# Optimization experiments

Measured on AMD Instinct MI355X. Metric: run time of the kernel, lower is better.

Reference implementation:

```python
import jax, jax.numpy as jnp
import numpy as np

# dims
B, T = 32, 512            # batch (cells), num TFs
G, PPG = 2000, 10         # num genes, cCRE peaks per gene (uniform cut)
P = G * PPG               # total peaks = 20000
E = 64000                 # PPI edges
NOUT = 10                 # output channels
GENE_DIM = 2              # GCNConv out dim


def setup_inputs() -> dict:
    key = jax.random.key(0)
    ks = jax.random.split(key, 8)
    x = jax.random.normal(ks[0], (B, T, P), jnp.float32)
    edge_index = jax.random.randint(ks[1], (2, E), 0, G, dtype=jnp.int32)
    # concatenation of all per-gene subNet fc1 weights: gene i uses W_sub[:, cut[i]:cut[i+1]]
    W_sub = jax.random.normal(ks[2], (T, P), jnp.float32) * 0.01
    b_sub = jnp.zeros((G,), jnp.float32)
    # PyG GCNConv lin.weight has shape [out=2, in=1]
    W_gcn = jax.random.normal(ks[3], (GENE_DIM, 1), jnp.float32)
    b_gcn = jnp.zeros((GENE_DIM,), jnp.float32)
    W_out = jax.random.normal(ks[4], (NOUT, G * GENE_DIM), jnp.float32) * 0.01
    b_out = jnp.zeros((NOUT,), jnp.float32)
    return dict(x=x, edge_index=edge_index, W_sub=W_sub, b_sub=b_sub,
                W_gcn=W_gcn, b_gcn=b_gcn, W_out=W_out, b_out=b_out)


def reference(x, edge_index, W_sub, b_sub, W_gcn, b_gcn, W_out, b_out):
    gene_seg = jnp.arange(P) // PPG  # peak -> gene id (uniform cut list)
    # block-diagonal tiny-FC loop fused: per-gene Linear(num_peak*num_tf -> 1)
    per_peak = jnp.einsum('btp,tp->bp', x, W_sub)                  # [B, P]
    h = jax.ops.segment_sum(per_peak.T, gene_seg, num_segments=G).T + b_sub  # [B, G]
    h = jax.nn.relu(h)                                              # cat_activate
    # GCNConv(1 -> 2), add_self_loops=False: xw = h W^T, then D^-1/2 A D^-1/2 agg
    xw = h[:, :, None] * W_gcn[:, 0][None, None, :]                # [B, G, 2]
    row, col = edge_index[0], edge_index[1]
    deg = jax.ops.segment_sum(jnp.ones((E,), x.dtype), col, num_segments=G)
    dinv = jnp.where(deg > 0, deg ** -0.5, 0.0)
    norm = dinv[row] * dinv[col]                                   # [E]
    msg = xw[:, row, :] * norm[None, :, None]                      # [B, E, 2]
    agg = jax.ops.segment_sum(msg.transpose(1, 0, 2), col,
                              num_segments=G).transpose(1, 0, 2) + b_gcn  # [B, G, 2]
    g = jax.nn.relu(agg).reshape(B, G * GENE_DIM)
    return g @ W_out.T + b_out                                     # [B, NOUT]
```

## Files before the change

kernel.cpp:

```cpp
#include <hip/hip_runtime.h>
#include <math.h>

#define BN    32
#define TN    512
#define GN    2000
#define PPGN  10
#define PN    (GN*PPGN)
#define EN    64000
#define NOUTN 10
#define PQN   (PN/4)

typedef float float4v __attribute__((ext_vector_type(4)));

__global__ __launch_bounds__(320)
void k_perpeak(const float* __restrict__ x,
               const float* __restrict__ W_sub,
               float* __restrict__ per_peak) {
    int idx = blockIdx.x * 320 + threadIdx.x;
    int b   = idx / PQN;
    int pq  = idx % PQN;

    const float4v* xp = (const float4v*)(x + (size_t)b * TN * PN) + pq;
    const float4v* wp = (const float4v*)W_sub + pq;

    float4v acc = {0.f, 0.f, 0.f, 0.f};
#pragma unroll 8
    for (int t = 0; t < TN; ++t) {
        float4v xv = __builtin_nontemporal_load(xp + (size_t)t * PQN);
        float4v wv = wp[(size_t)t * PQN];
        acc = xv * wv + acc;
    }

    float4v* pp = (float4v*)(per_peak + (size_t)b * PN) + pq;
    *pp = acc;
}

__global__ void k_h(const float* __restrict__ per_peak,
                    const float* __restrict__ b_sub,
                    float* __restrict__ h) {
    int idx = blockIdx.x * blockDim.x + threadIdx.x;
    if (idx >= BN * GN) return;
    int g = idx % GN, b = idx / GN;
    const float* pp = per_peak + (size_t)b * PN + g * PPGN;
    float s = b_sub[g];
#pragma unroll
    for (int k = 0; k < PPGN; ++k) s += pp[k];
    h[idx] = fmaxf(s, 0.0f);
}

__global__ void k_deg(const int* __restrict__ col, float* __restrict__ deg) {
    int e = blockIdx.x * blockDim.x + threadIdx.x;
    if (e < EN) atomicAdd(&deg[col[e]], 1.0f);
}

__global__ void k_dinv(const float* __restrict__ deg, float* __restrict__ dinv) {
    int g = blockIdx.x * blockDim.x + threadIdx.x;
    if (g < GN) {
        float d = deg[g];
        dinv[g] = (d > 0.0f) ? (1.0f / sqrtf(d)) : 0.0f;
    }
}

__global__ void k_s(const int* __restrict__ row, const int* __restrict__ col,
                    const float* __restrict__ dinv, const float* __restrict__ h,
                    float* __restrict__ s) {
    int idx = blockIdx.x * blockDim.x + threadIdx.x;
    if (idx >= EN * BN) return;
    int b = idx % BN;
    int e = idx / BN;
    int r = row[e], c = col[e];
    float nrm = dinv[r] * dinv[c];
    atomicAdd(&s[(size_t)b * GN + c], nrm * h[(size_t)b * GN + r]);
}

__global__ void k_out(const float* __restrict__ s,
                      const float* __restrict__ W_gcn,
                      const float* __restrict__ b_gcn,
                      const float* __restrict__ W_out,
                      const float* __restrict__ b_out,
                      float* __restrict__ out) {
    int b = blockIdx.x / NOUTN;
    int n = blockIdx.x % NOUTN;
    int lane = threadIdx.x;

    float w0 = W_gcn[0], w1 = W_gcn[1];
    float c0 = b_gcn[0], c1 = b_gcn[1];

    float acc = 0.0f;
    for (int g = lane; g < GN; g += 64) {
        float sv = s[(size_t)b * GN + g];
        float g0 = fmaxf(fmaf(sv, w0, c0), 0.0f);
        float g1 = fmaxf(fmaf(sv, w1, c1), 0.0f);
        const float* wo = &W_out[(size_t)n * (GN * 2) + 2 * g];
        acc = fmaf(g0, wo[0], acc);
        acc = fmaf(g1, wo[1], acc);
    }
#pragma unroll
    for (int off = 32; off > 0; off >>= 1)
        acc += __shfl_down(acc, off);
    if (lane == 0) out[b * NOUTN + n] = acc + b_out[n];
}

extern "C" void kernel_launch(void* const* d_in, const int* in_sizes, int n_in,
                              void* d_out, int out_size, void* d_ws, size_t ws_size,
                              hipStream_t stream) {
    const float* x         = (const float*)d_in[0];
    const int*   edge_index= (const int*)  d_in[1];
    const float* W_sub     = (const float*)d_in[2];
    const float* b_sub     = (const float*)d_in[3];
    const float* W_gcn     = (const float*)d_in[4];
    const float* b_gcn     = (const float*)d_in[5];
    const float* W_out     = (const float*)d_in[6];
    const float* b_out     = (const float*)d_in[7];
    float* out = (float*)d_out;

    char* ws = (char*)d_ws;
    float* per_peak = (float*)(ws);
    float* h        = (float*)(ws + 2560000);
    float* deg      = (float*)(ws + 2816000);
    float* dinv     = (float*)(ws + 2824000);
    float* s        = (float*)(ws + 2832000);

    const int* row = edge_index;
    const int* col = edge_index + EN;

    hipMemsetAsync(deg, 0, GN * sizeof(float), stream);
    hipMemsetAsync(s,   0, (size_t)BN * GN * sizeof(float), stream);

    k_perpeak<<<500, 320, 0, stream>>>(x, W_sub, per_peak);
    k_h      <<<((BN * GN) + 255) / 256, 256, 0, stream>>>(per_peak, b_sub, h);
    k_deg    <<<(EN + 255) / 256,        256, 0, stream>>>(col, deg);
    k_dinv   <<<(GN + 255) / 256,        256, 0, stream>>>(deg, dinv);
    k_s      <<<((EN * BN) + 255) / 256, 256, 0, stream>>>(row, col, dinv, h, s);
    k_out    <<<BN * NOUTN, 64, 0, stream>>>(s, W_gcn, b_gcn, W_out, b_out, out);
}
```

Before: 441.5 us.

## Reuse W_sub across four batches per thread and aggregate GCN in LDS

The per-peak kernel now has each thread handle four batch rows, so every W_sub load is reused four times. The grid shrinks to 160 blocks of 256 threads, which lowers occupancy and leaves fewer waves to hide latency while streaming x. The edge aggregation moves to one block per batch that accumulates into shared memory with LDS atomics, replacing global atomics and the memset of s. Each block walks all 64000 edges serially with only 256 threads, so the aggregation step now runs on just 32 blocks.

```diff
diff --git a/kernel.cpp b/kernel.cpp
--- a/kernel.cpp
+++ b/kernel.cpp
@@ -12,27 +12,39 @@
 
 typedef float float4v __attribute__((ext_vector_type(4)));
 
-__global__ __launch_bounds__(320)
+__global__ __launch_bounds__(256)
 void k_perpeak(const float* __restrict__ x,
                const float* __restrict__ W_sub,
                float* __restrict__ per_peak) {
-    int idx = blockIdx.x * 320 + threadIdx.x;
-    int b   = idx / PQN;
-    int pq  = idx % PQN;
+    int ptile = blockIdx.x;
+    int bg    = blockIdx.y;
+    int pq    = ptile * 256 + threadIdx.x;
+    if (pq >= PQN) return;
+    int b0 = bg * 4;
 
-    const float4v* xp = (const float4v*)(x + (size_t)b * TN * PN) + pq;
+    const float4v* xp = (const float4v*)x + (size_t)b0 * TN * PQN + pq;
     const float4v* wp = (const float4v*)W_sub + pq;
 
-    float4v acc = {0.f, 0.f, 0.f, 0.f};
-#pragma unroll 8
+    float4v acc0 = {0.f,0.f,0.f,0.f}, acc1 = {0.f,0.f,0.f,0.f};
+    float4v acc2 = {0.f,0.f,0.f,0.f}, acc3 = {0.f,0.f,0.f,0.f};
+#pragma unroll 4
     for (int t = 0; t < TN; ++t) {
-        float4v xv = __builtin_nontemporal_load(xp + (size_t)t * PQN);
         float4v wv = wp[(size_t)t * PQN];
-        acc = xv * wv + acc;
+        float4v x0 = __builtin_nontemporal_load(xp + (size_t)t * PQN);
+        float4v x1 = __builtin_nontemporal_load(xp + (size_t)(TN + t) * PQN);
+        float4v x2 = __builtin_nontemporal_load(xp + (size_t)(2 * TN + t) * PQN);
+        float4v x3 = __builtin_nontemporal_load(xp + (size_t)(3 * TN + t) * PQN);
+        acc0 = x0 * wv + acc0;
+        acc1 = x1 * wv + acc1;
+        acc2 = x2 * wv + acc2;
+        acc3 = x3 * wv + acc3;
     }
 
-    float4v* pp = (float4v*)(per_peak + (size_t)b * PN) + pq;
-    *pp = acc;
+    float4v* pp = (float4v*)per_peak + (size_t)b0 * PQN + pq;
+    pp[0]           = acc0;
+    pp[PQN]         = acc1;
+    pp[2 * PQN]     = acc2;
+    pp[3 * PQN]     = acc3;
 }
 
 __global__ void k_h(const float* __restrict__ per_peak,
@@ -61,16 +73,23 @@
     }
 }
 
-__global__ void k_s(const int* __restrict__ row, const int* __restrict__ col,
-                    const float* __restrict__ dinv, const float* __restrict__ h,
-                    float* __restrict__ s) {
-    int idx = blockIdx.x * blockDim.x + threadIdx.x;
-    if (idx >= EN * BN) return;
-    int b = idx % BN;
-    int e = idx / BN;
-    int r = row[e], c = col[e];
-    float nrm = dinv[r] * dinv[c];
-    atomicAdd(&s[(size_t)b * GN + c], nrm * h[(size_t)b * GN + r]);
+__global__ __launch_bounds__(256)
+void k_s(const int* __restrict__ row, const int* __restrict__ col,
+         const float* __restrict__ dinv, const float* __restrict__ h,
+         float* __restrict__ s) {
+    __shared__ float s_lds[GN];
+    int b = blockIdx.x;
+    for (int g = threadIdx.x; g < GN; g += 256) s_lds[g] = 0.0f;
+    __syncthreads();
+    const float* hb = h + (size_t)b * GN;
+    for (int e = threadIdx.x; e < EN; e += 256) {
+        int r = row[e], c = col[e];
+        float nrm = dinv[r] * dinv[c];
+        atomicAdd(&s_lds[c], nrm * hb[r]);
+    }
+    __syncthreads();
+    for (int g = threadIdx.x; g < GN; g += 256)
+        s[(size_t)b * GN + g] = s_lds[g];
 }
 
 __global__ void k_out(const float* __restrict__ s,
@@ -125,12 +144,12 @@
     const int* col = edge_index + EN;
 
     hipMemsetAsync(deg, 0, GN * sizeof(float), stream);
-    hipMemsetAsync(s,   0, (size_t)BN * GN * sizeof(float), stream);
 
-    k_perpeak<<<500, 320, 0, stream>>>(x, W_sub, per_peak);
+    dim3 grid_pp(20, 8);
+    k_perpeak<<<grid_pp, 256, 0, stream>>>(x, W_sub, per_peak);
     k_h      <<<((BN * GN) + 255) / 256, 256, 0, stream>>>(per_peak, b_sub, h);
     k_deg    <<<(EN + 255) / 256,        256, 0, stream>>>(col, deg);
     k_dinv   <<<(GN + 255) / 256,        256, 0, stream>>>(deg, dinv);
-    k_s      <<<((EN * BN) + 255) / 256, 256, 0, stream>>>(row, col, dinv, h, s);
+    k_s      <<<BN, 256, 0, stream>>>(row, col, dinv, h, s);
     k_out    <<<BN * NOUTN, 64, 0, stream>>>(s, W_gcn, b_gcn, W_out, b_out, out);
 }
```

Measured after the change: 472.3 us. 1.07x slower.
